# Performance work log

Hardware: AMD Instinct MI355X
Metric: run time of the kernel (lower is better)

Reference implementation:

```python
import jax, jax.numpy as jnp
import numpy as np

N_EXPERTS = 64
TOP_K = 2
LOAD_BALANCE_COEF = 0.01
D_MODEL = 4096
N_TOKENS = 16384


def setup_inputs() -> dict:
    key = jax.random.key(0)
    kx, kw = jax.random.split(key)
    x = jax.random.normal(kx, (N_TOKENS, D_MODEL), dtype=jnp.float32)
    # nn.init.normal_(gate.weight, std=0.01); shape (n_experts, d_model)
    gate_w = 0.01 * jax.random.normal(kw, (N_EXPERTS, D_MODEL), dtype=jnp.float32)
    return {"x": x, "gate_w": gate_w}


def reference(x, gate_w):
    # logits: (N, n_experts)
    logits = jnp.einsum('nd,ed->ne', x, gate_w)
    router_probs = jax.nn.softmax(logits, axis=-1)
    top_k_weights, top_k_indices = jax.lax.top_k(router_probs, TOP_K)
    routing_weights = top_k_weights / jnp.sum(top_k_weights, axis=-1, keepdims=True)
    top1 = top_k_indices[:, 0]
    one_hot = jax.nn.one_hot(top1, N_EXPERTS, dtype=x.dtype)  # (N, n_experts)
    f_i = jnp.mean(one_hot, axis=0)          # fraction of tokens per expert (detached)
    p_i = jnp.mean(router_probs, axis=0)     # mean router prob per expert (diff.)
    load_balance_loss = LOAD_BALANCE_COEF * jnp.sum(jax.lax.stop_gradient(f_i) * p_i)
    return routing_weights, top_k_indices, load_balance_loss
```

## Files before the change

kernel.cpp:

```cpp
#include <hip/hip_runtime.h>
#include <math.h>

#define N_TOKENS 16384
#define D_MODEL  4096
#define N_EXP    64

#define BK   16
#define LD   68
#define NW   8
#define KW   (D_MODEL / NW)
#define NT   (KW / BK)
#define NBLK (N_TOKENS / 64)

__global__ void __launch_bounds__(512)
router_fused(const float* __restrict__ x, const float* __restrict__ w,
             float* __restrict__ out, float* __restrict__ block_sums) {
    __shared__ float smem[NW * 4 * BK * LD];

    const int tid  = threadIdx.x;
    const int wv   = tid >> 6;
    const int lane = tid & 63;
    const int tok0 = blockIdx.x * 64;

    float* xs  = smem + wv * (4 * BK * LD);
    float* wsb = xs + 2 * BK * LD;

    const int srow = lane >> 2;
    const int skc  = (lane & 3) * 4;

    const int trow = (lane & 7) * 8;
    const int ecol = (lane >> 3) * 8;

    const float* xp = x + (size_t)(tok0 + srow) * D_MODEL + (size_t)wv * KW + skc;
    const float* wp = w + (size_t)srow * D_MODEL + (size_t)wv * KW + skc;

    float acc[8][8] = {};

#define LOADR(q, roff) (*(const float4*)((q) + (size_t)(roff) * D_MODEL))
#define STORE_TILE(buf, v, roff) do {                      \
        (buf)[(skc + 0) * LD + srow + (roff)] = (v).x;     \
        (buf)[(skc + 1) * LD + srow + (roff)] = (v).y;     \
        (buf)[(skc + 2) * LD + srow + (roff)] = (v).z;     \
        (buf)[(skc + 3) * LD + srow + (roff)] = (v).w;     \
    } while (0)

    {
        float4 a0 = LOADR(xp, 0),  a1 = LOADR(xp, 16);
        float4 a2 = LOADR(xp, 32), a3 = LOADR(xp, 48);
        float4 b0 = LOADR(wp, 0),  b1 = LOADR(wp, 16);
        float4 b2 = LOADR(wp, 32), b3 = LOADR(wp, 48);
        STORE_TILE(xs, a0, 0);  STORE_TILE(xs, a1, 16);
        STORE_TILE(xs, a2, 32); STORE_TILE(xs, a3, 48);
        STORE_TILE(wsb, b0, 0);  STORE_TILE(wsb, b1, 16);
        STORE_TILE(wsb, b2, 32); STORE_TILE(wsb, b3, 48);
    }

    auto compute_tile = [&](const float* xb, const float* wb) {
#pragma unroll
        for (int k = 0; k < BK; ++k) {
            const float* xr = xb + k * LD + trow;
            const float* wr = wb + k * LD + ecol;
            float4 xa = *(const float4*)xr;
            float4 xc = *(const float4*)(xr + 4);
            float4 wa = *(const float4*)wr;
            float4 wc = *(const float4*)(wr + 4);
            float xf[8] = {xa.x, xa.y, xa.z, xa.w, xc.x, xc.y, xc.z, xc.w};
            float wf[8] = {wa.x, wa.y, wa.z, wa.w, wc.x, wc.y, wc.z, wc.w};
#pragma unroll
            for (int i = 0; i < 8; ++i)
#pragma unroll
                for (int j = 0; j < 8; ++j)
                    acc[i][j] = fmaf(xf[i], wf[j], acc[i][j]);
        }
    };

#pragma unroll 2
    for (int t = 0; t < NT - 1; ++t) {
        float* xb = xs  + (t & 1) * (BK * LD);
        float* wb = wsb + (t & 1) * (BK * LD);
        float* xn = xs  + ((t + 1) & 1) * (BK * LD);
        float* wn = wsb + ((t + 1) & 1) * (BK * LD);

        const float* xq = xp + (t + 1) * BK;
        const float* wq = wp + (t + 1) * BK;
        float4 a0 = LOADR(xq, 0),  a1 = LOADR(xq, 16);
        float4 a2 = LOADR(xq, 32), a3 = LOADR(xq, 48);
        float4 b0 = LOADR(wq, 0),  b1 = LOADR(wq, 16);
        float4 b2 = LOADR(wq, 32), b3 = LOADR(wq, 48);

        compute_tile(xb, wb);

        STORE_TILE(xn, a0, 0);  STORE_TILE(xn, a1, 16);
        STORE_TILE(xn, a2, 32); STORE_TILE(xn, a3, 48);
        STORE_TILE(wn, b0, 0);  STORE_TILE(wn, b1, 16);
        STORE_TILE(wn, b2, 32); STORE_TILE(wn, b3, 48);
    }
    compute_tile(xs + ((NT - 1) & 1) * (BK * LD), wsb + ((NT - 1) & 1) * (BK * LD));

    __syncthreads();

    float* tile = smem + wv * 4096;
#pragma unroll
    for (int i = 0; i < 8; ++i) {
        *(float4*)&tile[(trow + i) * 64 + ecol] =
            make_float4(acc[i][0], acc[i][1], acc[i][2], acc[i][3]);
        *(float4*)&tile[(trow + i) * 64 + ecol + 4] =
            make_float4(acc[i][4], acc[i][5], acc[i][6], acc[i][7]);
    }
    __syncthreads();

    float p_acc = 0.f, f_acc = 0.f;
#pragma unroll 1
    for (int it = 0; it < 8; ++it) {
        const int tl = wv * 8 + it;
        const int o  = tl * 64 + lane;
        float logit = 0.f;
#pragma unroll
        for (int t8 = 0; t8 < NW; ++t8)
            logit += smem[t8 * 4096 + o];

        float m = logit;
#pragma unroll
        for (int off = 32; off; off >>= 1)
            m = fmaxf(m, __shfl_xor(m, off, 64));
        unsigned long long b1 = __ballot(logit == m);
        int i1 = __ffsll(b1) - 1;

        float p = expf(logit - m);
        float denom = p;
#pragma unroll
        for (int off = 32; off; off >>= 1)
            denom += __shfl_xor(denom, off, 64);

        p_acc += p / denom;
        if (lane == i1) f_acc += 1.f;

        float lx = (lane == i1) ? -__builtin_inff() : logit;
        float m2 = lx;
#pragma unroll
        for (int off = 32; off; off >>= 1)
            m2 = fmaxf(m2, __shfl_xor(m2, off, 64));
        unsigned long long b2 = __ballot(lx == m2);
        int i2 = __ffsll(b2) - 1;

        if (lane == 0) {
            float p1 = 1.0f / denom;
            float p2 = expf(m2 - m) / denom;
            float s12 = p1 + p2;
            int token = tok0 + tl;
            ((float2*)out)[token] = make_float2(p1 / s12, p2 / s12);
            ((float2*)(out + 2 * N_TOKENS))[token] =
                make_float2((float)i1, (float)i2);
        }
    }

    float* pf = smem + NW * 4096;
    pf[wv * 64 + lane]       = p_acc;
    pf[512 + wv * 64 + lane] = f_acc;
    __syncthreads();
    if (tid < N_EXP) {
        float ps = 0.f, fs = 0.f;
#pragma unroll
        for (int h = 0; h < NW; ++h) {
            ps += pf[h * 64 + tid];
            fs += pf[512 + h * 64 + tid];
        }
        block_sums[(size_t)blockIdx.x * 128 + tid]      = ps;
        block_sums[(size_t)blockIdx.x * 128 + 64 + tid] = fs;
    }
}

__global__ void __launch_bounds__(256)
router_final(const float* __restrict__ block_sums, float* __restrict__ out) {
    __shared__ float sp[4][N_EXP];
    __shared__ float sf[4][N_EXP];

    int tid  = threadIdx.x;
    int wv   = tid >> 6;
    int lane = tid & 63;

    float ps = 0.f, fs = 0.f;
#pragma unroll 8
    for (int b = wv * (NBLK / 4); b < (wv + 1) * (NBLK / 4); ++b) {
        ps += block_sums[(size_t)b * 128 + lane];
        fs += block_sums[(size_t)b * 128 + 64 + lane];
    }
    sp[wv][lane] = ps;
    sf[wv][lane] = fs;
    __syncthreads();

    if (tid < N_EXP) {
        float pt = sp[0][tid] + sp[1][tid] + sp[2][tid] + sp[3][tid];
        float ft = sf[0][tid] + sf[1][tid] + sf[2][tid] + sf[3][tid];
        float v = pt * ft;
#pragma unroll
        for (int off = 1; off < 64; off <<= 1)
            v += __shfl_xor(v, off, 64);
        if (tid == 0)
            out[4 * N_TOKENS] = 0.01f * v / ((float)N_TOKENS * (float)N_TOKENS);
    }
}

extern "C" void kernel_launch(void* const* d_in, const int* in_sizes, int n_in,
                              void* d_out, int out_size, void* d_ws, size_t ws_size,
                              hipStream_t stream) {
    (void)in_sizes; (void)n_in; (void)out_size; (void)ws_size;
    const float* x = (const float*)d_in[0];
    const float* w = (const float*)d_in[1];
    float* out = (float*)d_out;
    float* block_sums = (float*)d_ws;

    router_fused<<<NBLK, 512, 0, stream>>>(x, w, out, block_sums);
    router_final<<<1, 256, 0, stream>>>(block_sums, out);
}
```

Measured before the change: 432.7 us.

## Pre-transpose gate weights and read them directly from global, halving LDS

Adds a small kernel that transposes gate_w into a k-major layout in workspace. The main kernel then reads weight rows straight from global (L2-resident) instead of staging them through LDS, which halves shared memory per block and adds a launch bound aimed at higher occupancy. The cross-wave reduction now uses two phases over four LDS tiles because the old eight-tile scratch no longer fits. Risks include global load latency inside the inner FMA loop, reduced unrolling, and an extra kernel launch.

```diff
diff --git a/kernel.cpp b/kernel.cpp
--- a/kernel.cpp
+++ b/kernel.cpp
@@ -12,18 +12,41 @@
 #define NT   (KW / BK)
 #define NBLK (N_TOKENS / 64)
 
-__global__ void __launch_bounds__(512)
-router_fused(const float* __restrict__ x, const float* __restrict__ w,
+__global__ void __launch_bounds__(256)
+transpose_w(const float* __restrict__ w, float* __restrict__ wt) {
+    __shared__ float t[64][LD];
+    const int k0 = blockIdx.x * 64;
+    const int kc = (threadIdx.x & 15) * 4;
+    const int e0 = threadIdx.x >> 4;
+#pragma unroll
+    for (int p = 0; p < 4; ++p) {
+        int e = p * 16 + e0;
+        float4 v = *(const float4*)(w + (size_t)e * D_MODEL + k0 + kc);
+        t[kc + 0][e] = v.x; t[kc + 1][e] = v.y;
+        t[kc + 2][e] = v.z; t[kc + 3][e] = v.w;
+    }
+    __syncthreads();
+    const int kr = threadIdx.x >> 2;
+    const int ec = (threadIdx.x & 3) * 16;
+#pragma unroll
+    for (int j = 0; j < 4; ++j) {
+        float4 v = make_float4(t[kr][ec + j * 4 + 0], t[kr][ec + j * 4 + 1],
+                               t[kr][ec + j * 4 + 2], t[kr][ec + j * 4 + 3]);
+        *(float4*)(wt + (size_t)(k0 + kr) * N_EXP + ec + j * 4) = v;
+    }
+}
+
+__global__ void __launch_bounds__(512, 4)
+router_fused(const float* __restrict__ x, const float* __restrict__ wt,
              float* __restrict__ out, float* __restrict__ block_sums) {
-    __shared__ float smem[NW * 4 * BK * LD];
+    __shared__ float smem[NW * 2 * BK * LD];
 
     const int tid  = threadIdx.x;
     const int wv   = tid >> 6;
     const int lane = tid & 63;
     const int tok0 = blockIdx.x * 64;
 
-    float* xs  = smem + wv * (4 * BK * LD);
-    float* wsb = xs + 2 * BK * LD;
+    float* xs = smem + wv * (2 * BK * LD);
 
     const int srow = lane >> 2;
     const int skc  = (lane & 3) * 4;
@@ -32,7 +55,7 @@
     const int ecol = (lane >> 3) * 8;
 
     const float* xp = x + (size_t)(tok0 + srow) * D_MODEL + (size_t)wv * KW + skc;
-    const float* wp = w + (size_t)srow * D_MODEL + (size_t)wv * KW + skc;
+    const float* wp = wt + (size_t)wv * KW * N_EXP + ecol;
 
     float acc[8][8] = {};
 
@@ -47,21 +70,17 @@
     {
         float4 a0 = LOADR(xp, 0),  a1 = LOADR(xp, 16);
         float4 a2 = LOADR(xp, 32), a3 = LOADR(xp, 48);
-        float4 b0 = LOADR(wp, 0),  b1 = LOADR(wp, 16);
-        float4 b2 = LOADR(wp, 32), b3 = LOADR(wp, 48);
         STORE_TILE(xs, a0, 0);  STORE_TILE(xs, a1, 16);
         STORE_TILE(xs, a2, 32); STORE_TILE(xs, a3, 48);
-        STORE_TILE(wsb, b0, 0);  STORE_TILE(wsb, b1, 16);
-        STORE_TILE(wsb, b2, 32); STORE_TILE(wsb, b3, 48);
-    }
-
-    auto compute_tile = [&](const float* xb, const float* wb) {
-#pragma unroll
+    }
+
+    auto compute_tile = [&](const float* xb, int kbase) {
+#pragma unroll 4
         for (int k = 0; k < BK; ++k) {
             const float* xr = xb + k * LD + trow;
-            const float* wr = wb + k * LD + ecol;
             float4 xa = *(const float4*)xr;
             float4 xc = *(const float4*)(xr + 4);
+            const float* wr = wp + (size_t)(kbase + k) * N_EXP;
             float4 wa = *(const float4*)wr;
             float4 wc = *(const float4*)(wr + 4);
             float xf[8] = {xa.x, xa.y, xa.z, xa.w, xc.x, xc.y, xc.z, xc.w};
@@ -74,38 +93,45 @@
         }
     };
 
-#pragma unroll 2
     for (int t = 0; t < NT - 1; ++t) {
-        float* xb = xs  + (t & 1) * (BK * LD);
-        float* wb = wsb + (t & 1) * (BK * LD);
-        float* xn = xs  + ((t + 1) & 1) * (BK * LD);
-        float* wn = wsb + ((t + 1) & 1) * (BK * LD);
+        float* xb = xs + (t & 1) * (BK * LD);
+        float* xn = xs + ((t + 1) & 1) * (BK * LD);
 
         const float* xq = xp + (t + 1) * BK;
-        const float* wq = wp + (t + 1) * BK;
         float4 a0 = LOADR(xq, 0),  a1 = LOADR(xq, 16);
         float4 a2 = LOADR(xq, 32), a3 = LOADR(xq, 48);
-        float4 b0 = LOADR(wq, 0),  b1 = LOADR(wq, 16);
-        float4 b2 = LOADR(wq, 32), b3 = LOADR(wq, 48);
-
-        compute_tile(xb, wb);
+
+        compute_tile(xb, t * BK);
 
         STORE_TILE(xn, a0, 0);  STORE_TILE(xn, a1, 16);
         STORE_TILE(xn, a2, 32); STORE_TILE(xn, a3, 48);
-        STORE_TILE(wn, b0, 0);  STORE_TILE(wn, b1, 16);
-        STORE_TILE(wn, b2, 32); STORE_TILE(wn, b3, 48);
-    }
-    compute_tile(xs + ((NT - 1) & 1) * (BK * LD), wsb + ((NT - 1) & 1) * (BK * LD));
-
-    __syncthreads();
-
-    float* tile = smem + wv * 4096;
-#pragma unroll
-    for (int i = 0; i < 8; ++i) {
-        *(float4*)&tile[(trow + i) * 64 + ecol] =
-            make_float4(acc[i][0], acc[i][1], acc[i][2], acc[i][3]);
-        *(float4*)&tile[(trow + i) * 64 + ecol + 4] =
-            make_float4(acc[i][4], acc[i][5], acc[i][6], acc[i][7]);
+    }
+    compute_tile(xs + ((NT - 1) & 1) * (BK * LD), (NT - 1) * BK);
+
+    __syncthreads();
+
+    float* tile = smem + (wv & 3) * 4096;
+    if (wv < 4) {
+#pragma unroll
+        for (int i = 0; i < 8; ++i) {
+            *(float4*)&tile[(trow + i) * 64 + ecol] =
+                make_float4(acc[i][0], acc[i][1], acc[i][2], acc[i][3]);
+            *(float4*)&tile[(trow + i) * 64 + ecol + 4] =
+                make_float4(acc[i][4], acc[i][5], acc[i][6], acc[i][7]);
+        }
+    }
+    __syncthreads();
+    if (wv >= 4) {
+#pragma unroll
+        for (int i = 0; i < 8; ++i) {
+            float4* tp = (float4*)&tile[(trow + i) * 64 + ecol];
+            float4 v0 = tp[0], v1 = tp[1];
+            v0.x += acc[i][0]; v0.y += acc[i][1];
+            v0.z += acc[i][2]; v0.w += acc[i][3];
+            v1.x += acc[i][4]; v1.y += acc[i][5];
+            v1.z += acc[i][6]; v1.w += acc[i][7];
+            tp[0] = v0; tp[1] = v1;
+        }
     }
     __syncthreads();
 
@@ -114,10 +140,7 @@
     for (int it = 0; it < 8; ++it) {
         const int tl = wv * 8 + it;
         const int o  = tl * 64 + lane;
-        float logit = 0.f;
-#pragma unroll
-        for (int t8 = 0; t8 < NW; ++t8)
-            logit += smem[t8 * 4096 + o];
+        float logit = smem[o] + smem[4096 + o] + smem[8192 + o] + smem[12288 + o];
 
         float m = logit;
 #pragma unroll
@@ -154,7 +177,7 @@
         }
     }
 
-    float* pf = smem + NW * 4096;
+    float* pf = smem + 4 * 4096;
     pf[wv * 64 + lane]       = p_acc;
     pf[512 + wv * 64 + lane] = f_acc;
     __syncthreads();
@@ -208,8 +231,11 @@
     const float* x = (const float*)d_in[0];
     const float* w = (const float*)d_in[1];
     float* out = (float*)d_out;
-    float* block_sums = (float*)d_ws;
-
-    router_fused<<<NBLK, 512, 0, stream>>>(x, w, out, block_sums);
+
+    float* wT = (float*)d_ws;
+    float* block_sums = wT + (size_t)D_MODEL * N_EXP;
+
+    transpose_w<<<D_MODEL / 64, 256, 0, stream>>>(w, wT);
+    router_fused<<<NBLK, 512, 0, stream>>>(x, wT, out, block_sums);
     router_final<<<1, 256, 0, stream>>>(block_sums, out);
 }
```

New measurement: 500.3 us. 15.6% more time.
